# Kernel optimization log

Measured on AMD Instinct MI355X. Metric: run time of the kernel, lower is better.

Reference implementation:

```python
import jax, jax.numpy as jnp
import numpy as np

EPS = 1e-6
NUM_HEADS = 16


def _layernorm(x, g, b):
    m = jnp.mean(x, axis=-1, keepdims=True)
    v = jnp.mean(jnp.square(x - m), axis=-1, keepdims=True)
    return (x - m) / jnp.sqrt(v + EPS) * g + b


def _rotate_half(x):
    x1, x2 = jnp.split(x, 2, axis=-1)
    return jnp.concatenate([-x2, x1], axis=-1)


def setup_inputs() -> dict:
    key = jax.random.key(0)
    B, N, C = 2, 2048, 1024
    H = NUM_HEADS
    D = C // H
    F = int(C * 4.0)
    ks = jax.random.split(key, 12)
    s = 0.02
    pos = jnp.arange(N)[:, None].astype(jnp.float32)
    inv_freq = 1.0 / (10000.0 ** (jnp.arange(0, D, 2, dtype=jnp.float32) / D))
    freqs = pos * inv_freq[None, :]          # [N, D/2]
    emb = jnp.concatenate([freqs, freqs], axis=-1)  # [N, D]
    return {
        "x": jax.random.normal(ks[0], (B, N, C), jnp.float32),
        "rotary_cos": jnp.cos(emb),
        "rotary_sin": jnp.sin(emb),
        "ln1_g": jnp.ones((C,), jnp.float32),
        "ln1_b": jnp.zeros((C,), jnp.float32),
        "Wq": jax.random.normal(ks[1], (C, C), jnp.float32) * s,
        "bq": jnp.zeros((C,), jnp.float32),
        "Wk": jax.random.normal(ks[2], (C, C), jnp.float32) * s,
        "bk": jnp.zeros((C,), jnp.float32),
        "Wv": jax.random.normal(ks[3], (C, C), jnp.float32) * s,
        "bv": jnp.zeros((C,), jnp.float32),
        "Wo": jax.random.normal(ks[4], (C, C), jnp.float32) * s,
        "bo": jnp.zeros((C,), jnp.float32),
        "ln2_g": jnp.ones((C,), jnp.float32),
        "ln2_b": jnp.zeros((C,), jnp.float32),
        "W1": jax.random.normal(ks[5], (F, C), jnp.float32) * s,
        "b1": jnp.zeros((F,), jnp.float32),
        "W2": jax.random.normal(ks[6], (C, F), jnp.float32) * s,
        "b2": jnp.zeros((C,), jnp.float32),
    }


def reference(x, rotary_cos, rotary_sin, ln1_g, ln1_b, Wq, bq, Wk, bk, Wv, bv,
              Wo, bo, ln2_g, ln2_b, W1, b1, W2, b2):
    B, N, C = x.shape
    H = NUM_HEADS
    D = C // H

    # --- attention branch ---
    h = _layernorm(x, ln1_g, ln1_b)
    q = (h @ Wq.T + bq).reshape(B, N, H, D).transpose(0, 2, 1, 3)  # [B,H,N,D]
    k = (h @ Wk.T + bk).reshape(B, N, H, D).transpose(0, 2, 1, 3)
    v = (h @ Wv.T + bv).reshape(B, N, H, D).transpose(0, 2, 1, 3)

    cos = rotary_cos[None, None, :, :]  # [1,1,N,D]
    sin = rotary_sin[None, None, :, :]
    q = q * cos + _rotate_half(q) * sin
    k = k * cos + _rotate_half(k) * sin

    scale = D ** -0.5
    attn = jnp.einsum('bhnd,bhmd->bhnm', q, k) * scale
    attn = jax.nn.softmax(attn, axis=-1)
    out = jnp.einsum('bhnm,bhmd->bhnd', attn, v)
    out = out.transpose(0, 2, 1, 3).reshape(B, N, C)
    out = out @ Wo.T + bo
    x = x + out

    # --- MLP branch ---
    h = _layernorm(x, ln2_g, ln2_b)
    h = jax.nn.gelu(h @ W1.T + b1, approximate=False)  # torch nn.GELU exact
    h = h @ W2.T + b2
    return x + h
```

## Files before the change

### kernel.cpp

```cpp
#include <hip/hip_runtime.h>
#include <hip/hip_bf16.h>

#define B_ 2
#define N_ 2048
#define C_ 1024
#define H_ 16
#define D_ 64
#define F_ 4096
#define M_ 4096

typedef __attribute__((ext_vector_type(8))) short bf16x8;
typedef __attribute__((ext_vector_type(4))) float f32x4;

__device__ inline unsigned short f2bf(float f) {
  unsigned int u = __float_as_uint(f);
  u = (u + 0x7FFFu + ((u >> 16) & 1u)) >> 16;
  return (unsigned short)u;
}

__global__ __launch_bounds__(256)
void cvt_all(const float4* __restrict__ s0, const float4* __restrict__ s1,
             const float4* __restrict__ s2, const float4* __restrict__ s3,
             const float4* __restrict__ s4, const float4* __restrict__ s5,
             ushort4* __restrict__ d0, ushort4* __restrict__ d1,
             ushort4* __restrict__ d2, ushort4* __restrict__ d3,
             ushort4* __restrict__ d4, ushort4* __restrict__ d5) {
  int b = blockIdx.x;
  const float4* s; ushort4* d; int i;
  if      (b < 1024) { s = s0; d = d0; i = b * 256 + threadIdx.x; }
  else if (b < 2048) { s = s1; d = d1; i = (b - 1024) * 256 + threadIdx.x; }
  else if (b < 3072) { s = s2; d = d2; i = (b - 2048) * 256 + threadIdx.x; }
  else if (b < 4096) { s = s3; d = d3; i = (b - 3072) * 256 + threadIdx.x; }
  else if (b < 8192) { s = s4; d = d4; i = (b - 4096) * 256 + threadIdx.x; }
  else               { s = s5; d = d5; i = (b - 8192) * 256 + threadIdx.x; }
  float4 f = s[i];
  ushort4 o;
  o.x = f2bf(f.x); o.y = f2bf(f.y); o.z = f2bf(f.z); o.w = f2bf(f.w);
  d[i] = o;
}

__global__ __launch_bounds__(256)
void ln_kernel(const float* __restrict__ x, const float* __restrict__ g,
               const float* __restrict__ b, unsigned short* __restrict__ out) {
  __shared__ float red[8];
  const int row = blockIdx.x;
  const int t = threadIdx.x;
  const float4 xv = *(const float4*)(x + row * 1024 + t * 4);
  float s  = xv.x + xv.y + xv.z + xv.w;
  float sq = xv.x * xv.x + xv.y * xv.y + xv.z * xv.z + xv.w * xv.w;
  #pragma unroll
  for (int off = 32; off >= 1; off >>= 1) {
    s  += __shfl_down(s, off);
    sq += __shfl_down(sq, off);
  }
  const int lane = t & 63, wave = t >> 6;
  if (lane == 0) { red[wave * 2] = s; red[wave * 2 + 1] = sq; }
  __syncthreads();
  float ts = red[0] + red[2] + red[4] + red[6];
  float tq = red[1] + red[3] + red[5] + red[7];
  float mean = ts * (1.0f / 1024.0f);
  float var  = tq * (1.0f / 1024.0f) - mean * mean;
  float rstd = rsqrtf(var + 1e-6f);
  float xs[4] = {xv.x, xv.y, xv.z, xv.w};
  #pragma unroll
  for (int i = 0; i < 4; i++) {
    int c = t * 4 + i;
    float y = (xs[i] - mean) * rstd * g[c] + b[c];
    out[row * 1024 + c] = f2bf(y);
  }
}

template<int MODE, int BN>
__global__ __launch_bounds__(256)
void gemm_bt(const unsigned short* __restrict__ A,
             const unsigned short* __restrict__ Bw,
             int K, int Nout, int npc,
             const float* __restrict__ bias,
             const float* __restrict__ resid,
             unsigned short* __restrict__ out_bf,
             float* __restrict__ out_f32) {
  constexpr int NJ = BN / 32;
  __shared__ unsigned short sA[2][128 * 64];
  __shared__ unsigned short sB[2][BN * 64];
  const int t = threadIdx.x;
  const int wave = t >> 6, lane = t & 63;
  const int quad = lane >> 4, l16 = lane & 15;
  const int wm = (wave & 1) * 64, wn = (wave >> 1) * (BN / 2);
  const int id = blockIdx.y * gridDim.x + blockIdx.x;
  const int xcd = id & 7, r_ = id >> 3;
  const int n_blk = xcd * npc + r_ % npc;
  const int m_blk = r_ / npc;
  const int m0 = m_blk * 128, n0 = n_blk * BN;

  f32x4 acc[4][NJ];
  #pragma unroll
  for (int i = 0; i < 4; i++)
    #pragma unroll
    for (int j = 0; j < NJ; j++) acc[i][j] = (f32x4){0.f, 0.f, 0.f, 0.f};

  const unsigned short* gA = A  + (m0 + (t >> 3)) * K + (t & 7) * 8;
  const unsigned short* gB = Bw + (n0 + (t >> 3)) * K + (t & 7) * 8;

  auto stage = [&](int k0, int buf) {
    unsigned short* lA = &sA[buf][(wave * 8) * 64];
    unsigned short* lB = &sB[buf][(wave * 8) * 64];
    #pragma unroll
    for (int i = 0; i < 4; i++)
      __builtin_amdgcn_global_load_lds((const unsigned int*)(gA + (32 * i) * K + k0),
                                       (unsigned int*)(lA + 32 * i * 64), 16, 0, 0);
    #pragma unroll
    for (int i = 0; i < BN / 32; i++)
      __builtin_amdgcn_global_load_lds((const unsigned int*)(gB + (32 * i) * K + k0),
                                       (unsigned int*)(lB + 32 * i * 64), 16, 0, 0);
  };

  stage(0, 0);
  __syncthreads();

  const int nk = K >> 6;
  for (int kt = 0; kt < nk; kt++) {
    const int cur = kt & 1;
    if (kt + 1 < nk) stage((kt + 1) * 64, cur ^ 1);
    #pragma unroll
    for (int kk = 0; kk < 2; kk++) {
      bf16x8 af[4], bfr[NJ];
      #pragma unroll
      for (int i = 0; i < 4; i++)
        af[i] = *(const bf16x8*)(&sA[cur][(wm + i * 16 + l16) * 64 + kk * 32 + quad * 8]);
      #pragma unroll
      for (int j = 0; j < NJ; j++)
        bfr[j] = *(const bf16x8*)(&sB[cur][(wn + j * 16 + l16) * 64 + kk * 32 + quad * 8]);
      #pragma unroll
      for (int i = 0; i < 4; i++)
        #pragma unroll
        for (int j = 0; j < NJ; j++)
          acc[i][j] = __builtin_amdgcn_mfma_f32_16x16x32_bf16(af[i], bfr[j], acc[i][j], 0, 0, 0);
    }
    __syncthreads();
  }

  #pragma unroll
  for (int i = 0; i < 4; i++) {
    #pragma unroll
    for (int j = 0; j < NJ; j++) {
      int col = n0 + wn + j * 16 + l16;
      #pragma unroll
      for (int r = 0; r < 4; r++) {
        int row = m0 + wm + i * 16 + quad * 4 + r;
        float v = acc[i][j][r];
        if (MODE == 1 || MODE == 3) {
          out_f32[row * Nout + col] = v + bias[col] + resid[row * Nout + col];
        } else {
          v += bias[col];
          float w = v * (1.0f + 0.044715f * v * v);
          float gl = v / (1.0f + __expf(-1.5957691216f * w));
          out_bf[row * Nout + col] = f2bf(gl);
        }
      }
    }
  }
}

__global__ __launch_bounds__(256)
void gemm_qkv(const unsigned short* __restrict__ A,
              const unsigned short* __restrict__ Bw,
              const float* __restrict__ bq, const float* __restrict__ bk,
              const float* __restrict__ bv,
              const float* __restrict__ rc, const float* __restrict__ rs,
              unsigned short* __restrict__ qo, unsigned short* __restrict__ ko,
              unsigned short* __restrict__ vt) {
  const int K = C_;
  __shared__ unsigned short sA[2][128 * 64];
  __shared__ unsigned short sB[2][128 * 64];
  const int t = threadIdx.x;
  const int wave = t >> 6, lane = t & 63;
  const int quad = lane >> 4, l16 = lane & 15;
  const int wm = (wave & 1) * 64, wn = (wave >> 1) * 64;
  const int id = blockIdx.y * gridDim.x + blockIdx.x;
  const int xcd = id & 7, r_ = id >> 3;
  const int n_blk = xcd * 3 + r_ % 3;
  const int m_blk = r_ / 3;
  const int m0 = m_blk * 128, n0 = n_blk * 128;

  f32x4 acc[4][4];
  #pragma unroll
  for (int i = 0; i < 4; i++)
    #pragma unroll
    for (int j = 0; j < 4; j++) acc[i][j] = (f32x4){0.f, 0.f, 0.f, 0.f};

  const unsigned short* gA = A  + (m0 + (t >> 3)) * K + (t & 7) * 8;
  const unsigned short* gB = Bw + (n0 + (t >> 3)) * K + (t & 7) * 8;

  auto stage = [&](int k0, int buf) {
    unsigned short* lA = &sA[buf][(wave * 8) * 64];
    unsigned short* lB = &sB[buf][(wave * 8) * 64];
    #pragma unroll
    for (int i = 0; i < 4; i++) {
      __builtin_amdgcn_global_load_lds((const unsigned int*)(gA + (32 * i) * K + k0),
                                       (unsigned int*)(lA + 32 * i * 64), 16, 0, 0);
      __builtin_amdgcn_global_load_lds((const unsigned int*)(gB + (32 * i) * K + k0),
                                       (unsigned int*)(lB + 32 * i * 64), 16, 0, 0);
    }
  };

  stage(0, 0);
  __syncthreads();

  const int nk = K >> 6;
  for (int kt = 0; kt < nk; kt++) {
    const int cur = kt & 1;
    if (kt + 1 < nk) stage((kt + 1) * 64, cur ^ 1);
    #pragma unroll
    for (int kk = 0; kk < 2; kk++) {
      bf16x8 af[4], bfr[4];
      #pragma unroll
      for (int i = 0; i < 4; i++)
        af[i] = *(const bf16x8*)(&sA[cur][(wm + i * 16 + l16) * 64 + kk * 32 + quad * 8]);
      #pragma unroll
      for (int j = 0; j < 4; j++)
        bfr[j] = *(const bf16x8*)(&sB[cur][(wn + j * 16 + l16) * 64 + kk * 32 + quad * 8]);
      #pragma unroll
      for (int i = 0; i < 4; i++)
        #pragma unroll
        for (int j = 0; j < 4; j++)
          acc[i][j] = __builtin_amdgcn_mfma_f32_16x16x32_bf16(af[i], bfr[j], acc[i][j], 0, 0, 0);
    }
    __syncthreads();
  }

  const int rgn = n_blk >> 3;
  const int c0 = (n_blk & 7) * 128;

  if (rgn == 2) {
    #pragma unroll
    for (int i = 0; i < 4; i++) {
      int row0 = m0 + wm + i * 16 + quad * 4;
      int bidx = row0 >> 11, n0r = row0 & 2047;
      #pragma unroll
      for (int j = 0; j < 4; j++) {
        int d = j * 16 + l16;
        int c = c0 + wn + d;
        int h = c >> 6;
        float bb = bv[c];
        __hip_bfloat162 p01 = __float22bfloat162_rn(float2{acc[i][j][0] + bb, acc[i][j][1] + bb});
        __hip_bfloat162 p23 = __float22bfloat162_rn(float2{acc[i][j][2] + bb, acc[i][j][3] + bb});
        unsigned int u01, u23;
        __builtin_memcpy(&u01, &p01, 4);
        __builtin_memcpy(&u23, &p23, 4);
        *(uint2*)(vt + (((bidx * 16 + h) * 64) + (c & 63)) * 2048 + n0r) = make_uint2(u01, u23);
      }
    }
  } else {
    const float* bias = (rgn == 0) ? bq : bk;
    unsigned short* outp = (rgn == 0) ? qo : ko;
    #pragma unroll
    for (int i = 0; i < 4; i++) {
      #pragma unroll
      for (int r = 0; r < 4; r++) {
        int row = m0 + wm + i * 16 + quad * 4 + r;
        int bidx = row >> 11, n = row & 2047;
        #pragma unroll
        for (int j = 0; j < 4; j++) {
          int d = j * 16 + l16;
          int c = c0 + wn + d;
          int h = c >> 6;
          int oi = ((bidx * 16 + h) * 2048 + n) * 64 + d;
          float val = acc[i][j][r] + bias[c];
          float pv  = acc[i][j ^ 2][r] + bias[c ^ 32];
          float rot = (j < 2) ? -pv : pv;
          float y = val * rc[n * 64 + d] + rot * rs[n * 64 + d];
          if (rgn == 0) y *= 0.125f;
          outp[oi] = f2bf(y);
        }
      }
    }
  }
}

__global__ __launch_bounds__(256)
void flash_attn(const unsigned short* __restrict__ q,
                const unsigned short* __restrict__ k,
                const unsigned short* __restrict__ vt,
                unsigned short* __restrict__ o) {
  __shared__ unsigned short sK[2][64 * 64];
  __shared__ unsigned short sVt[2][64 * 64];
  __shared__ unsigned short sPt[2][4][16 * 72];
  const int t = threadIdx.x;
  const int wave = t >> 6, lane = t & 63;
  const int quad = lane >> 4, l16 = lane & 15;
  const int id = blockIdx.y * gridDim.x + blockIdx.x;
  const int bh = (id & 7) * 4 + ((id >> 3) & 3);
  const int qb = id >> 5;
  const int base = bh * (N_ * D_);

  bf16x8 qa[2][2];
  #pragma unroll
  for (int qt = 0; qt < 2; qt++) {
    int qrow = qb * 128 + wave * 32 + qt * 16 + l16;
    #pragma unroll
    for (int kk = 0; kk < 2; kk++)
      qa[qt][kk] = *(const bf16x8*)(q + base + qrow * D_ + kk * 32 + quad * 8);
  }
  float l_i[2] = {0.f, 0.f};
  f32x4 o_acc[2][4];
  #pragma unroll
  for (int qt = 0; qt < 2; qt++)
    #pragma unroll
    for (int dt = 0; dt < 4; dt++) o_acc[qt][dt] = (f32x4){0.f, 0.f, 0.f, 0.f};

  const unsigned short* gK  = k  + base + (t >> 3) * 64 + (t & 7) * 8;
  const unsigned short* gVt = vt + bh * (64 * 2048) + (t >> 3) * 2048 + (t & 7) * 8;

  auto stage = [&](int kt, int buf) {
    unsigned short* lK = &sK[buf][(wave * 8) * 64];
    unsigned short* lV = &sVt[buf][(wave * 8) * 64];
    #pragma unroll
    for (int i = 0; i < 2; i++) {
      __builtin_amdgcn_global_load_lds((const unsigned int*)(gK + (kt * 64 + 32 * i) * 64),
                                       (unsigned int*)(lK + 32 * i * 64), 16, 0, 0);
      __builtin_amdgcn_global_load_lds((const unsigned int*)(gVt + 32 * i * 2048 + kt * 64),
                                       (unsigned int*)(lV + 32 * i * 64), 16, 0, 0);
    }
  };
  stage(0, 0);
  __syncthreads();

  for (int kt = 0; kt < N_ / 64; kt++) {
    const int cur = kt & 1;
    if (kt < N_ / 64 - 1) stage(kt + 1, cur ^ 1);

    f32x4 s_acc[2][4];
    #pragma unroll
    for (int nt = 0; nt < 4; nt++) {
      bf16x8 kb0 = *(const bf16x8*)(&sK[cur][(nt * 16 + l16) * 64 + quad * 8]);
      bf16x8 kb1 = *(const bf16x8*)(&sK[cur][(nt * 16 + l16) * 64 + 32 + quad * 8]);
      #pragma unroll
      for (int qt = 0; qt < 2; qt++) {
        f32x4 a = (f32x4){0.f, 0.f, 0.f, 0.f};
        a = __builtin_amdgcn_mfma_f32_16x16x32_bf16(kb0, qa[qt][0], a, 0, 0, 0);
        a = __builtin_amdgcn_mfma_f32_16x16x32_bf16(kb1, qa[qt][1], a, 0, 0, 0);
        s_acc[qt][nt] = a;
      }
    }
    #pragma unroll
    for (int qt = 0; qt < 2; qt++) {
      float rsum = 0.f;
      #pragma unroll
      for (int nt = 0; nt < 4; nt++)
        #pragma unroll
        for (int r = 0; r < 4; r++) {
          float p = __expf(s_acc[qt][nt][r]);
          s_acc[qt][nt][r] = p;
          rsum += p;
        }
      rsum += __shfl_xor(rsum, 16);
      rsum += __shfl_xor(rsum, 32);
      l_i[qt] += rsum;
      #pragma unroll
      for (int nt = 0; nt < 4; nt++) {
        __hip_bfloat162 p01 = __float22bfloat162_rn(float2{s_acc[qt][nt][0], s_acc[qt][nt][1]});
        __hip_bfloat162 p23 = __float22bfloat162_rn(float2{s_acc[qt][nt][2], s_acc[qt][nt][3]});
        unsigned int u01, u23;
        __builtin_memcpy(&u01, &p01, 4);
        __builtin_memcpy(&u23, &p23, 4);
        *(uint2*)(&sPt[qt][wave][l16 * 72 + nt * 16 + quad * 4]) = make_uint2(u01, u23);
      }
    }
    __asm__ volatile("s_waitcnt lgkmcnt(0)" ::: "memory");
    bf16x8 pt[2][2];
    #pragma unroll
    for (int qt = 0; qt < 2; qt++) {
      pt[qt][0] = *(const bf16x8*)(&sPt[qt][wave][l16 * 72 + quad * 8]);
      pt[qt][1] = *(const bf16x8*)(&sPt[qt][wave][l16 * 72 + 32 + quad * 8]);
    }
    #pragma unroll
    for (int dt = 0; dt < 4; dt++) {
      int d0 = dt * 16 + l16;
      bf16x8 va0 = *(const bf16x8*)(&sVt[cur][d0 * 64 + quad * 8]);
      bf16x8 va1 = *(const bf16x8*)(&sVt[cur][d0 * 64 + 32 + quad * 8]);
      #pragma unroll
      for (int qt = 0; qt < 2; qt++) {
        o_acc[qt][dt] = __builtin_amdgcn_mfma_f32_16x16x32_bf16(va0, pt[qt][0], o_acc[qt][dt], 0, 0, 0);
        o_acc[qt][dt] = __builtin_amdgcn_mfma_f32_16x16x32_bf16(va1, pt[qt][1], o_acc[qt][dt], 0, 0, 0);
      }
    }
    __syncthreads();
  }

  const int b = bh >> 4, h = bh & 15;
  #pragma unroll
  for (int qt = 0; qt < 2; qt++) {
    const float inv = 1.0f / l_i[qt];
    const int tok = b * N_ + qb * 128 + wave * 32 + qt * 16 + l16;
    #pragma unroll
    for (int dt = 0; dt < 4; dt++) {
      __hip_bfloat162 p01 = __float22bfloat162_rn(float2{o_acc[qt][dt][0] * inv, o_acc[qt][dt][1] * inv});
      __hip_bfloat162 p23 = __float22bfloat162_rn(float2{o_acc[qt][dt][2] * inv, o_acc[qt][dt][3] * inv});
      unsigned int u01, u23;
      __builtin_memcpy(&u01, &p01, 4);
      __builtin_memcpy(&u23, &p23, 4);
      int col = h * 64 + dt * 16 + quad * 4;
      *(uint2*)(o + tok * C_ + col) = make_uint2(u01, u23);
    }
  }
}

extern "C" void kernel_launch(void* const* d_in, const int* in_sizes, int n_in,
                              void* d_out, int out_size, void* d_ws, size_t ws_size,
                              hipStream_t stream) {
  const float* x   = (const float*)d_in[0];
  const float* rc  = (const float*)d_in[1];
  const float* rs  = (const float*)d_in[2];
  const float* g1  = (const float*)d_in[3];
  const float* be1 = (const float*)d_in[4];
  const float* Wq  = (const float*)d_in[5];
  const float* bq  = (const float*)d_in[6];
  const float* Wk  = (const float*)d_in[7];
  const float* bk  = (const float*)d_in[8];
  const float* Wv  = (const float*)d_in[9];
  const float* bv  = (const float*)d_in[10];
  const float* Wo  = (const float*)d_in[11];
  const float* bo  = (const float*)d_in[12];
  const float* g2  = (const float*)d_in[13];
  const float* be2 = (const float*)d_in[14];
  const float* W1  = (const float*)d_in[15];
  const float* b1m = (const float*)d_in[16];
  const float* W2  = (const float*)d_in[17];
  const float* b2m = (const float*)d_in[18];
  float* out = (float*)d_out;

  char* ws = (char*)d_ws;
  unsigned short* wqkv = (unsigned short*)(ws + 0);
  unsigned short* wo   = (unsigned short*)(ws + 6291456);
  unsigned short* w1   = (unsigned short*)(ws + 8388608);
  unsigned short* w2   = (unsigned short*)(ws + 16777216);
  unsigned short* h1   = (unsigned short*)(ws + 25165824);
  unsigned short* qa   = (unsigned short*)(ws + 33554432);
  unsigned short* ka   = (unsigned short*)(ws + 41943040);
  unsigned short* va   = (unsigned short*)(ws + 50331648);
  unsigned short* ao   = (unsigned short*)(ws + 58720256);
  float*          x1   = (float*)(ws + 67108864);
  unsigned short* u    = (unsigned short*)(ws + 33554432);

  cvt_all<<<12288, 256, 0, stream>>>(
      (const float4*)Wq, (const float4*)Wk, (const float4*)Wv, (const float4*)Wo,
      (const float4*)W1, (const float4*)W2,
      (ushort4*)wqkv, (ushort4*)(wqkv + 1048576), (ushort4*)(wqkv + 2097152),
      (ushort4*)wo, (ushort4*)w1, (ushort4*)w2);

  ln_kernel<<<4096, 256, 0, stream>>>(x, g1, be1, h1);
  gemm_qkv<<<dim3(24, 32), 256, 0, stream>>>(h1, wqkv, bq, bk, bv, rc, rs, qa, ka, va);
  flash_attn<<<dim3(16, 32), 256, 0, stream>>>(qa, ka, va, ao);
  gemm_bt<1, 64><<<dim3(16, 32), 256, 0, stream>>>(ao, wo, 1024, 1024, 2, bo, x, nullptr, x1);
  ln_kernel<<<4096, 256, 0, stream>>>(x1, g2, be2, h1);
  gemm_bt<2, 64><<<dim3(64, 32), 256, 0, stream>>>(h1, w1, 1024, 4096, 8, b1m, nullptr, u, nullptr);
  gemm_bt<3, 64><<<dim3(16, 32), 256, 0, stream>>>(u, w2, 4096, 1024, 2, b2m, x1, nullptr, out);
}
```

Before: 428.2 us.

## Use 256x256 tiles with 512-thread blocks for QKV and FC1 GEMMs

Replaces the 128x128-tile QKV GEMM and the generic FC1+GELU GEMM with dedicated kernels that use 256x256 output tiles, 8 waves per block and 128x64 per-wave subtiles. The XCD-aware block mapping is changed so blocks sharing the same B or A panel land on the same XCD. Larger tiles raise arithmetic intensity and cut global/L2 traffic, but they need 128KB LDS and more accumulator registers per block. The grid also shrinks to 192 and 256 blocks, which may underfill the 256 CUs.

```diff
diff --git a/kernel.cpp b/kernel.cpp
--- a/kernel.cpp
+++ b/kernel.cpp
@@ -161,30 +161,28 @@
   }
 }
 
-__global__ __launch_bounds__(256)
-void gemm_qkv(const unsigned short* __restrict__ A,
-              const unsigned short* __restrict__ Bw,
-              const float* __restrict__ bq, const float* __restrict__ bk,
-              const float* __restrict__ bv,
-              const float* __restrict__ rc, const float* __restrict__ rs,
-              unsigned short* __restrict__ qo, unsigned short* __restrict__ ko,
-              unsigned short* __restrict__ vt) {
-  const int K = C_;
-  __shared__ unsigned short sA[2][128 * 64];
-  __shared__ unsigned short sB[2][128 * 64];
+
+__global__ __launch_bounds__(512, 2)
+void gemm_gelu256(const unsigned short* __restrict__ A,
+                  const unsigned short* __restrict__ Bw,
+                  const float* __restrict__ bias,
+                  unsigned short* __restrict__ out_bf) {
+  const int K = 1024, Nout = 4096;
+  __shared__ unsigned short sA[2][256 * 64];
+  __shared__ unsigned short sB[2][256 * 64];
   const int t = threadIdx.x;
   const int wave = t >> 6, lane = t & 63;
   const int quad = lane >> 4, l16 = lane & 15;
-  const int wm = (wave & 1) * 64, wn = (wave >> 1) * 64;
-  const int id = blockIdx.y * gridDim.x + blockIdx.x;
+  const int wm = (wave & 1) * 128, wn = (wave >> 1) * 64;
+  const int id = blockIdx.x;
   const int xcd = id & 7, r_ = id >> 3;
-  const int n_blk = xcd * 3 + r_ % 3;
-  const int m_blk = r_ / 3;
-  const int m0 = m_blk * 128, n0 = n_blk * 128;
-
-  f32x4 acc[4][4];
-  #pragma unroll
-  for (int i = 0; i < 4; i++)
+  const int n_blk = xcd * 2 + (r_ >> 4);
+  const int m_blk = r_ & 15;
+  const int m0 = m_blk * 256, n0 = n_blk * 256;
+
+  f32x4 acc[8][4];
+  #pragma unroll
+  for (int i = 0; i < 8; i++)
     #pragma unroll
     for (int j = 0; j < 4; j++) acc[i][j] = (f32x4){0.f, 0.f, 0.f, 0.f};
 
@@ -196,10 +194,10 @@
     unsigned short* lB = &sB[buf][(wave * 8) * 64];
     #pragma unroll
     for (int i = 0; i < 4; i++) {
-      __builtin_amdgcn_global_load_lds((const unsigned int*)(gA + (32 * i) * K + k0),
-                                       (unsigned int*)(lA + 32 * i * 64), 16, 0, 0);
-      __builtin_amdgcn_global_load_lds((const unsigned int*)(gB + (32 * i) * K + k0),
-                                       (unsigned int*)(lB + 32 * i * 64), 16, 0, 0);
+      __builtin_amdgcn_global_load_lds((const unsigned int*)(gA + (64 * i) * K + k0),
+                                       (unsigned int*)(lA + 64 * i * 64), 16, 0, 0);
+      __builtin_amdgcn_global_load_lds((const unsigned int*)(gB + (64 * i) * K + k0),
+                                       (unsigned int*)(lB + 64 * i * 64), 16, 0, 0);
     }
   };
 
@@ -212,15 +210,15 @@
     if (kt + 1 < nk) stage((kt + 1) * 64, cur ^ 1);
     #pragma unroll
     for (int kk = 0; kk < 2; kk++) {
-      bf16x8 af[4], bfr[4];
-      #pragma unroll
-      for (int i = 0; i < 4; i++)
+      bf16x8 af[8], bfr[4];
+      #pragma unroll
+      for (int i = 0; i < 8; i++)
         af[i] = *(const bf16x8*)(&sA[cur][(wm + i * 16 + l16) * 64 + kk * 32 + quad * 8]);
       #pragma unroll
       for (int j = 0; j < 4; j++)
         bfr[j] = *(const bf16x8*)(&sB[cur][(wn + j * 16 + l16) * 64 + kk * 32 + quad * 8]);
       #pragma unroll
-      for (int i = 0; i < 4; i++)
+      for (int i = 0; i < 8; i++)
         #pragma unroll
         for (int j = 0; j < 4; j++)
           acc[i][j] = __builtin_amdgcn_mfma_f32_16x16x32_bf16(af[i], bfr[j], acc[i][j], 0, 0, 0);
@@ -228,12 +226,97 @@
     __syncthreads();
   }
 
-  const int rgn = n_blk >> 3;
-  const int c0 = (n_blk & 7) * 128;
+  #pragma unroll
+  for (int i = 0; i < 8; i++) {
+    #pragma unroll
+    for (int j = 0; j < 4; j++) {
+      int col = n0 + wn + j * 16 + l16;
+      float bb = bias[col];
+      #pragma unroll
+      for (int r = 0; r < 4; r++) {
+        int row = m0 + wm + i * 16 + quad * 4 + r;
+        float v = acc[i][j][r] + bb;
+        float w = v * (1.0f + 0.044715f * v * v);
+        float gl = v / (1.0f + __expf(-1.5957691216f * w));
+        out_bf[row * Nout + col] = f2bf(gl);
+      }
+    }
+  }
+}
+
+__global__ __launch_bounds__(512, 2)
+void gemm_qkv256(const unsigned short* __restrict__ A,
+                 const unsigned short* __restrict__ Bw,
+                 const float* __restrict__ bq, const float* __restrict__ bk,
+                 const float* __restrict__ bv,
+                 const float* __restrict__ rc, const float* __restrict__ rs,
+                 unsigned short* __restrict__ qo, unsigned short* __restrict__ ko,
+                 unsigned short* __restrict__ vt) {
+  const int K = C_;
+  __shared__ unsigned short sA[2][256 * 64];
+  __shared__ unsigned short sB[2][256 * 64];
+  const int t = threadIdx.x;
+  const int wave = t >> 6, lane = t & 63;
+  const int quad = lane >> 4, l16 = lane & 15;
+  const int wm = (wave & 1) * 128, wn = (wave >> 1) * 64;
+  const int id = blockIdx.x;
+  const int xcd = id & 7, r_ = id >> 3;
+  const int m_blk = xcd * 2 + r_ / 12;
+  const int n_blk = r_ % 12;
+  const int m0 = m_blk * 256, n0 = n_blk * 256;
+
+  f32x4 acc[8][4];
+  #pragma unroll
+  for (int i = 0; i < 8; i++)
+    #pragma unroll
+    for (int j = 0; j < 4; j++) acc[i][j] = (f32x4){0.f, 0.f, 0.f, 0.f};
+
+  const unsigned short* gA = A  + (m0 + (t >> 3)) * K + (t & 7) * 8;
+  const unsigned short* gB = Bw + (n0 + (t >> 3)) * K + (t & 7) * 8;
+
+  auto stage = [&](int k0, int buf) {
+    unsigned short* lA = &sA[buf][(wave * 8) * 64];
+    unsigned short* lB = &sB[buf][(wave * 8) * 64];
+    #pragma unroll
+    for (int i = 0; i < 4; i++) {
+      __builtin_amdgcn_global_load_lds((const unsigned int*)(gA + (64 * i) * K + k0),
+                                       (unsigned int*)(lA + 64 * i * 64), 16, 0, 0);
+      __builtin_amdgcn_global_load_lds((const unsigned int*)(gB + (64 * i) * K + k0),
+                                       (unsigned int*)(lB + 64 * i * 64), 16, 0, 0);
+    }
+  };
+
+  stage(0, 0);
+  __syncthreads();
+
+  const int nk = K >> 6;
+  for (int kt = 0; kt < nk; kt++) {
+    const int cur = kt & 1;
+    if (kt + 1 < nk) stage((kt + 1) * 64, cur ^ 1);
+    #pragma unroll
+    for (int kk = 0; kk < 2; kk++) {
+      bf16x8 af[8], bfr[4];
+      #pragma unroll
+      for (int i = 0; i < 8; i++)
+        af[i] = *(const bf16x8*)(&sA[cur][(wm + i * 16 + l16) * 64 + kk * 32 + quad * 8]);
+      #pragma unroll
+      for (int j = 0; j < 4; j++)
+        bfr[j] = *(const bf16x8*)(&sB[cur][(wn + j * 16 + l16) * 64 + kk * 32 + quad * 8]);
+      #pragma unroll
+      for (int i = 0; i < 8; i++)
+        #pragma unroll
+        for (int j = 0; j < 4; j++)
+          acc[i][j] = __builtin_amdgcn_mfma_f32_16x16x32_bf16(af[i], bfr[j], acc[i][j], 0, 0, 0);
+    }
+    __syncthreads();
+  }
+
+  const int rgn = n_blk >> 2;
+  const int c0 = (n_blk & 3) * 256;
 
   if (rgn == 2) {
     #pragma unroll
-    for (int i = 0; i < 4; i++) {
+    for (int i = 0; i < 8; i++) {
       int row0 = m0 + wm + i * 16 + quad * 4;
       int bidx = row0 >> 11, n0r = row0 & 2047;
       #pragma unroll
@@ -247,14 +330,14 @@
         unsigned int u01, u23;
         __builtin_memcpy(&u01, &p01, 4);
         __builtin_memcpy(&u23, &p23, 4);
-        *(uint2*)(vt + (((bidx * 16 + h) * 64) + (c & 63)) * 2048 + n0r) = make_uint2(u01, u23);
+        *(uint2*)(vt + (((bidx * 16 + h) * 64) + d) * 2048 + n0r) = make_uint2(u01, u23);
       }
     }
   } else {
     const float* bias = (rgn == 0) ? bq : bk;
     unsigned short* outp = (rgn == 0) ? qo : ko;
     #pragma unroll
-    for (int i = 0; i < 4; i++) {
+    for (int i = 0; i < 8; i++) {
       #pragma unroll
       for (int r = 0; r < 4; r++) {
         int row = m0 + wm + i * 16 + quad * 4 + r;
@@ -449,10 +532,10 @@
       (ushort4*)wo, (ushort4*)w1, (ushort4*)w2);
 
   ln_kernel<<<4096, 256, 0, stream>>>(x, g1, be1, h1);
-  gemm_qkv<<<dim3(24, 32), 256, 0, stream>>>(h1, wqkv, bq, bk, bv, rc, rs, qa, ka, va);
+  gemm_qkv256<<<192, 512, 0, stream>>>(h1, wqkv, bq, bk, bv, rc, rs, qa, ka, va);
   flash_attn<<<dim3(16, 32), 256, 0, stream>>>(qa, ka, va, ao);
   gemm_bt<1, 64><<<dim3(16, 32), 256, 0, stream>>>(ao, wo, 1024, 1024, 2, bo, x, nullptr, x1);
   ln_kernel<<<4096, 256, 0, stream>>>(x1, g2, be2, h1);
-  gemm_bt<2, 64><<<dim3(64, 32), 256, 0, stream>>>(h1, w1, 1024, 4096, 8, b1m, nullptr, u, nullptr);
+  gemm_gelu256<<<256, 512, 0, stream>>>(h1, w1, b1m, u);
   gemm_bt<3, 64><<<dim3(16, 32), 256, 0, stream>>>(u, w2, 4096, 1024, 2, b2m, x1, nullptr, out);
 }
```

New measurement: 406.9 us. -5.0%, faster.
